# Optimization experiments

Hardware: AMD Instinct MI355X
Metric: run time of the kernel (lower is better)

The kernel has to match this reference:

```python
import jax, jax.numpy as jnp
import numpy as np

KH, KW = 11, 11
H, W = 6144, 6144


def setup_inputs() -> dict:
    key = jax.random.key(0)
    k1, k2 = jax.random.split(key)
    X = jax.random.normal(k1, (H, W), dtype=jnp.float32)
    weight = jax.random.uniform(k2, (KH, KW), dtype=jnp.float32)
    bias = jnp.zeros((1,), dtype=jnp.float32)
    return {"X": X, "weight": weight, "bias": bias}


def reference(X, weight, bias):
    # valid 2D cross-correlation: out[i,j] = sum(X[i:i+kh, j:j+kw] * K) + bias
    lhs = X[None, None]            # (1, 1, H, W)
    rhs = weight[None, None]       # (1, 1, kh, kw)  cross-correlation (no flip)
    out = jax.lax.conv_general_dilated(
        lhs, rhs,
        window_strides=(1, 1),
        padding="VALID",
        dimension_numbers=("NCHW", "OIHW", "NCHW"),
    )[0, 0]                         # (H-kh+1, W-kw+1)
    return out + bias[0]
```

## Files before the change

kernel.cpp:

```cpp
#include <hip/hip_runtime.h>

typedef _Float16 half8 __attribute__((ext_vector_type(8)));
typedef __fp16  fp16x2 __attribute__((ext_vector_type(2)));
typedef float f32x4 __attribute__((ext_vector_type(4)));

#define HH 6144
#define WW 6144
#define KH 11
#define KW 11
#define OH (HH - KH + 1)
#define OW (WW - KW + 1)

#define BROWS 32
#define BCOLS 128
#define SR 42
#define SCH 40
#define ROWB 640
#define A_TASKS 1680
#define A_PAD 1728
#define B_TASKS 704
#define TOT_WAVETASKS 38
#define B_OFF 27648
#define LDSB 38912
#define CV_TASKS 840

#define TILES_X 48
#define TILES_Y 192
#define NWG (TILES_X * TILES_Y)

__global__ void build_B_kernel(const float* __restrict__ Wt,
                               _Float16* __restrict__ Bp) {
    const int t = (int)blockIdx.x * 256 + (int)threadIdx.x;
    if (t < 11 * 64 * 8) {
        const int e  = t & 7;
        const int l  = (t >> 3) & 63;
        const int kb = t >> 9;
        const int n  = l & 15;
        const int q  = (l >> 4) * 8 + e;
        const int d  = q - n;
        float v = (d >= 0 && d < KW) ? Wt[kb * KW + d] : 0.f;
        Bp[t] = (_Float16)v;
    }
}

union pk2 { fp16x2 h; unsigned int u; };
static __device__ __forceinline__ unsigned int cvt2(float a, float b) {
#if defined(__has_builtin) && __has_builtin(__builtin_amdgcn_cvt_pkrtz)
    pk2 r; r.h = __builtin_amdgcn_cvt_pkrtz(a, b);
#else
    pk2 r; r.h[0] = (__fp16)a; r.h[1] = (__fp16)b;
#endif
    return r.u;
}

__global__ __launch_bounds__(256, 4)
void conv2d_dma2_kernel(const float* __restrict__ X,
                        const _Float16* __restrict__ Bp,
                        const float* __restrict__ bias,
                        float* __restrict__ out)
{
    __shared__ __align__(16) char lds[LDSB];

    const int bid = (int)blockIdx.x;
    const int sb  = (bid & 7) * (NWG / 8) + (bid >> 3);
    const int txt = sb % TILES_X;
    const int tyt = sb / TILES_X;

    const int x0 = txt * BCOLS;
    const int y0 = tyt * BROWS;
    const int tid = (int)threadIdx.x;
    const int lane = tid & 63;
    const int wv = tid >> 6;
    const int n  = lane & 15;
    const int h  = lane >> 4;
    const int rt = wv & 1;
    const int cs = wv >> 1;
    const float bv = bias[0];

    const bool interior = (txt < TILES_X - 1) && (tyt < TILES_Y - 1);

    if (interior) {
        #pragma unroll
        for (int k = 0; k < 10; ++k) {
            const int wabs = k * 4 + wv;
            if (wabs < TOT_WAVETASKS) {
                char* ldst = lds + wabs * 1024;
                const void* src;
                if (wabs < 27) {
                    const int t = wabs * 64 + lane;
                    int r = t / SCH;
                    const int j = t - r * SCH;
                    if (r > SR - 1) r = SR - 1;
                    src = (const void*)(X + (size_t)(y0 + r) * WW + (x0 + 4 * j));
                } else {
                    const int tb = (wabs - 27) * 64 + lane;
                    src = (const void*)((const char*)Bp + (size_t)tb * 16);
                }
                __builtin_amdgcn_global_load_lds(
                    (const __attribute__((address_space(1))) void*)src,
                    (__attribute__((address_space(3))) void*)ldst,
                    16, 0, 0);
            }
        }
    } else {
        #pragma unroll 1
        for (int k = 0; k < 10; ++k) {
            const int wabs = k * 4 + wv;
            if (wabs < TOT_WAVETASKS) {
                const int t = wabs * 64 + lane;
                if (wabs < 27) {
                    int r = t / SCH;
                    const int j = t - r * SCH;
                    if (r > SR - 1) r = SR - 1;
                    const int gy = y0 + r;
                    const int gx = x0 + 4 * j;
                    f32x4 v = {0.f, 0.f, 0.f, 0.f};
                    if (gy < HH) {
                        const float* rp = X + (size_t)gy * WW;
                        if (gx + 3 < WW) {
                            v = *reinterpret_cast<const f32x4*>(rp + gx);
                        } else {
                            if (gx + 0 < WW) v[0] = rp[gx + 0];
                            if (gx + 1 < WW) v[1] = rp[gx + 1];
                            if (gx + 2 < WW) v[2] = rp[gx + 2];
                        }
                    }
                    *reinterpret_cast<f32x4*>(lds + (size_t)t * 16) = v;
                } else {
                    const int tb = t - A_PAD;
                    *reinterpret_cast<uint4*>(lds + (size_t)t * 16) =
                        *reinterpret_cast<const uint4*>((const char*)Bp + (size_t)tb * 16);
                }
            }
        }
    }

    __syncthreads();

    f32x4 CV[4][2];
    #pragma unroll
    for (int it = 0; it < 4; ++it) {
        const int idx = it * 256 + tid;
        if (idx < CV_TASKS) {
            const int r = idx / 20;
            const int m = idx - r * 20;
            const char* frow = lds + (size_t)(r * SCH + 2 * m) * 16;
            CV[it][0] = *reinterpret_cast<const f32x4*>(frow);
            CV[it][1] = *reinterpret_cast<const f32x4*>(frow + 16);
        }
    }

    __syncthreads();

    #pragma unroll
    for (int it = 0; it < 4; ++it) {
        const int idx = it * 256 + tid;
        if (idx < CV_TASKS) {
            const int r = idx / 20;
            const int m = idx - r * 20;
            union { unsigned int u[4]; uint4 q; } fr;
            fr.u[0] = cvt2(CV[it][0][0], CV[it][0][1]);
            fr.u[1] = cvt2(CV[it][0][2], CV[it][0][3]);
            fr.u[2] = cvt2(CV[it][1][0], CV[it][1][1]);
            fr.u[3] = cvt2(CV[it][1][2], CV[it][1][3]);
            *reinterpret_cast<uint4*>(
                lds + (size_t)r * ROWB + (r & 7) * 32 + m * 16) = fr.q;
        }
    }

    f32x4 acc[4];
    #pragma unroll
    for (int c = 0; c < 4; ++c) acc[c] = (f32x4){bv, bv, bv, bv};

    __syncthreads();

    const char* abase = lds + (16 * rt + n) * ROWB + 128 * cs + 16 * h;
    const char* bbase = lds + B_OFF + lane * 16;
    #pragma unroll
    for (int kb = 0; kb < 11; ++kb) {
        const half8 bf = *reinterpret_cast<const half8*>(bbase + kb * 1024);
        const char* arow = abase + kb * ROWB + ((n + kb) & 7) * 32;
        #pragma unroll
        for (int c = 0; c < 4; ++c) {
            half8 a = *reinterpret_cast<const half8*>(arow + 32 * c);
            acc[c] = __builtin_amdgcn_mfma_f32_16x16x32_f16(a, bf, acc[c], 0, 0, 0);
        }
    }

    const int orow0 = y0 + 16 * rt + 4 * h;
    const int ocol0 = x0 + 64 * cs + n;
    if (interior) {
        #pragma unroll
        for (int r = 0; r < 4; ++r) {
            float* op = out + (size_t)(orow0 + r) * OW + ocol0;
            #pragma unroll
            for (int c = 0; c < 4; ++c)
                op[16 * c] = acc[c][r];
        }
    } else {
        #pragma unroll
        for (int r = 0; r < 4; ++r) {
            if (orow0 + r < OH) {
                float* op = out + (size_t)(orow0 + r) * OW + ocol0;
                #pragma unroll
                for (int c = 0; c < 4; ++c)
                    if (ocol0 + 16 * c < OW) op[16 * c] = acc[c][r];
            }
        }
    }
}

extern "C" void kernel_launch(void* const* d_in, const int* in_sizes, int n_in,
                              void* d_out, int out_size, void* d_ws, size_t ws_size,
                              hipStream_t stream) {
    const float* X    = (const float*)d_in[0];
    const float* Wt   = (const float*)d_in[1];
    const float* bias = (const float*)d_in[2];
    float* out        = (float*)d_out;
    _Float16* Bp      = (_Float16*)d_ws;

    build_B_kernel<<<dim3(22), dim3(256), 0, stream>>>(Wt, Bp);
    conv2d_dma2_kernel<<<dim3(NWG), dim3(256), 0, stream>>>(X, Bp, bias, out);
}
```

Measured before the change: 76.07 us.

## Compact Toeplitz weight layout and trim halo staging to cut LDS footprint

Replaces the per-lane expanded B fragment (1 KB per kernel row) with a compact 40-slot sliding Toeplitz layout where each lane reads at offset (8h-n+15). The input staging is narrowed from 40 to 36 float4 chunks per row (144 columns, enough for 128+10), shrinking LDS from about 38 KB to 31 KB. Together these allow raising launch bounds from 4 to 5 workgroups per CU to improve occupancy and latency hiding. The unaligned per-lane B reads may cause LDS bank conflicts.

```diff
diff --git a/kernel.cpp b/kernel.cpp
--- a/kernel.cpp
+++ b/kernel.cpp
@@ -14,32 +14,35 @@
 #define BROWS 32
 #define BCOLS 128
 #define SR 42
-#define SCH 40
-#define ROWB 640
-#define A_TASKS 1680
-#define A_PAD 1728
-#define B_TASKS 704
-#define TOT_WAVETASKS 38
-#define B_OFF 27648
-#define LDSB 38912
-#define CV_TASKS 840
+#define SCH 36
+#define ROWB 576
+#define A_TASKS 1512
+#define A_PAD 1536
+#define B_SLOTS 448
+#define B_BYTES 7168
+#define TOT_WAVETASKS 31
+#define B_OFF 24576
+#define LDSB 31744
+#define CV_TASKS 756
 
 #define TILES_X 48
 #define TILES_Y 192
 #define NWG (TILES_X * TILES_Y)
 
 __global__ void build_B_kernel(const float* __restrict__ Wt,
-                               _Float16* __restrict__ Bp) {
+                               _Float16* __restrict__ Bc) {
     const int t = (int)blockIdx.x * 256 + (int)threadIdx.x;
-    if (t < 11 * 64 * 8) {
-        const int e  = t & 7;
-        const int l  = (t >> 3) & 63;
-        const int kb = t >> 9;
-        const int n  = l & 15;
-        const int q  = (l >> 4) * 8 + e;
-        const int d  = q - n;
-        float v = (d >= 0 && d < KW) ? Wt[kb * KW + d] : 0.f;
-        Bp[t] = (_Float16)v;
+    if (t < B_SLOTS * 8) {
+        const int e    = t & 7;
+        const int slot = t >> 3;
+        const int kb   = slot / 40;
+        const int s    = slot - kb * 40;
+        float v = 0.f;
+        if (kb < KH) {
+            const int d = s + e - 15;
+            if (d >= 0 && d < KW) v = Wt[kb * KW + d];
+        }
+        Bc[t] = (_Float16)v;
     }
 }
 
@@ -53,9 +56,9 @@
     return r.u;
 }
 
-__global__ __launch_bounds__(256, 4)
-void conv2d_dma2_kernel(const float* __restrict__ X,
-                        const _Float16* __restrict__ Bp,
+__global__ __launch_bounds__(256, 5)
+void conv2d_dma3_kernel(const float* __restrict__ X,
+                        const _Float16* __restrict__ Bc,
                         const float* __restrict__ bias,
                         float* __restrict__ out)
 {
@@ -81,20 +84,20 @@
 
     if (interior) {
         #pragma unroll
-        for (int k = 0; k < 10; ++k) {
+        for (int k = 0; k < 8; ++k) {
             const int wabs = k * 4 + wv;
             if (wabs < TOT_WAVETASKS) {
                 char* ldst = lds + wabs * 1024;
                 const void* src;
-                if (wabs < 27) {
+                if (wabs < 24) {
                     const int t = wabs * 64 + lane;
                     int r = t / SCH;
                     const int j = t - r * SCH;
                     if (r > SR - 1) r = SR - 1;
                     src = (const void*)(X + (size_t)(y0 + r) * WW + (x0 + 4 * j));
                 } else {
-                    const int tb = (wabs - 27) * 64 + lane;
-                    src = (const void*)((const char*)Bp + (size_t)tb * 16);
+                    const int tb = (wabs - 24) * 64 + lane;
+                    src = (const void*)((const char*)Bc + (size_t)tb * 16);
                 }
                 __builtin_amdgcn_global_load_lds(
                     (const __attribute__((address_space(1))) void*)src,
@@ -104,11 +107,11 @@
         }
     } else {
         #pragma unroll 1
-        for (int k = 0; k < 10; ++k) {
+        for (int k = 0; k < 8; ++k) {
             const int wabs = k * 4 + wv;
             if (wabs < TOT_WAVETASKS) {
                 const int t = wabs * 64 + lane;
-                if (wabs < 27) {
+                if (wabs < 24) {
                     int r = t / SCH;
                     const int j = t - r * SCH;
                     if (r > SR - 1) r = SR - 1;
@@ -129,7 +132,7 @@
                 } else {
                     const int tb = t - A_PAD;
                     *reinterpret_cast<uint4*>(lds + (size_t)t * 16) =
-                        *reinterpret_cast<const uint4*>((const char*)Bp + (size_t)tb * 16);
+                        *reinterpret_cast<const uint4*>((const char*)Bc + (size_t)tb * 16);
                 }
             }
         }
@@ -137,13 +140,13 @@
 
     __syncthreads();
 
-    f32x4 CV[4][2];
-    #pragma unroll
-    for (int it = 0; it < 4; ++it) {
+    f32x4 CV[3][2];
+    #pragma unroll
+    for (int it = 0; it < 3; ++it) {
         const int idx = it * 256 + tid;
         if (idx < CV_TASKS) {
-            const int r = idx / 20;
-            const int m = idx - r * 20;
+            const int r = idx / 18;
+            const int m = idx - r * 18;
             const char* frow = lds + (size_t)(r * SCH + 2 * m) * 16;
             CV[it][0] = *reinterpret_cast<const f32x4*>(frow);
             CV[it][1] = *reinterpret_cast<const f32x4*>(frow + 16);
@@ -153,11 +156,11 @@
     __syncthreads();
 
     #pragma unroll
-    for (int it = 0; it < 4; ++it) {
+    for (int it = 0; it < 3; ++it) {
         const int idx = it * 256 + tid;
         if (idx < CV_TASKS) {
-            const int r = idx / 20;
-            const int m = idx - r * 20;
+            const int r = idx / 18;
+            const int m = idx - r * 18;
             union { unsigned int u[4]; uint4 q; } fr;
             fr.u[0] = cvt2(CV[it][0][0], CV[it][0][1]);
             fr.u[1] = cvt2(CV[it][0][2], CV[it][0][3]);
@@ -175,10 +178,10 @@
     __syncthreads();
 
     const char* abase = lds + (16 * rt + n) * ROWB + 128 * cs + 16 * h;
-    const char* bbase = lds + B_OFF + lane * 16;
+    const char* bbase = lds + B_OFF + (8 * h - n + 15) * 16;
     #pragma unroll
     for (int kb = 0; kb < 11; ++kb) {
-        const half8 bf = *reinterpret_cast<const half8*>(bbase + kb * 1024);
+        const half8 bf = *reinterpret_cast<const half8*>(bbase + kb * 640);
         const char* arow = abase + kb * ROWB + ((n + kb) & 7) * 32;
         #pragma unroll
         for (int c = 0; c < 4; ++c) {
@@ -217,8 +220,8 @@
     const float* Wt   = (const float*)d_in[1];
     const float* bias = (const float*)d_in[2];
     float* out        = (float*)d_out;
-    _Float16* Bp      = (_Float16*)d_ws;
-
-    build_B_kernel<<<dim3(22), dim3(256), 0, stream>>>(Wt, Bp);
-    conv2d_dma2_kernel<<<dim3(NWG), dim3(256), 0, stream>>>(X, Bp, bias, out);
-}
+    _Float16* Bc      = (_Float16*)d_ws;
+
+    build_B_kernel<<<dim3(14), dim3(256), 0, stream>>>(Wt, Bc);
+    conv2d_dma3_kernel<<<dim3(NWG), dim3(256), 0, stream>>>(X, Bc, bias, out);
+}
```

Result: faster. 72.20 us (-5.1%).
